# Optimization experiments

Hardware: AMD Instinct MI355X
Metric: run time of the kernel (lower is better)

The kernel has to match this reference:

```python
import jax, jax.numpy as jnp
import numpy as np

NUM_HEADS = 8  # from init_kwargs

def _conv1x1(x, W, b):
    # x: [B, Cin, H, W], W: [Cout, Cin], b: [Cout]  (nn.Conv2d kernel_size=1)
    return jnp.einsum('bchw,oc->bohw', x, W) + b[None, :, None, None]

def setup_inputs() -> dict:
    key = jax.random.key(0)
    ks = jax.random.split(key, 9)
    B, C, H, W = 8, 256, 32, 32
    Ck, Cv, Co = 256, 256, 256
    s = 1.0 / np.sqrt(C)
    return {
        'x':  jax.random.normal(ks[0], (B, C, H, W), dtype=jnp.float32),
        'Wq': jax.random.normal(ks[1], (Ck, C), dtype=jnp.float32) * s,
        'bq': jax.random.normal(ks[2], (Ck,), dtype=jnp.float32) * 0.02,
        'Wk': jax.random.normal(ks[3], (Ck, C), dtype=jnp.float32) * s,
        'bk': jax.random.normal(ks[4], (Ck,), dtype=jnp.float32) * 0.02,
        'Wv': jax.random.normal(ks[5], (Cv, C), dtype=jnp.float32) * s,
        'bv': jax.random.normal(ks[6], (Cv,), dtype=jnp.float32) * 0.02,
        'Wo': jax.random.normal(ks[7], (Co, Cv), dtype=jnp.float32) * s,
        'bo': jax.random.normal(ks[8], (Co,), dtype=jnp.float32) * 0.02,
    }

def reference(x, Wq, bq, Wk, bk, Wv, bv, Wo, bo):
    B, C, H, W = x.shape
    q = _conv1x1(x, Wq, bq)  # [B, Ck, H, W]
    k = _conv1x1(x, Wk, bk)  # [B, Ck, H, W]
    v = _conv1x1(x, Wv, bv)  # [B, Cv, H, W]
    nh = NUM_HEADS
    dk = q.shape[1] // nh
    dv = v.shape[1] // nh
    N = H * W
    # split heads, flatten spatial dims into sequence
    q = q.reshape(B, nh, dk, N) * (dk ** -0.5)
    k = k.reshape(B, nh, dk, N)
    v = v.reshape(B, nh, dv, N)
    logits = jnp.einsum('bhdn,bhdm->bhnm', q, k)        # [B, nh, N, N]
    attn = jax.nn.softmax(logits, axis=-1)
    o = jnp.einsum('bhnm,bhdm->bhdn', attn, v)           # [B, nh, dv, N]
    o = o.reshape(B, nh * dv, H, W)
    return _conv1x1(o, Wo, bo)                           # [B, Co, H, W]
```

## Files before the change

kernel.cpp:

```cpp
#include <hip/hip_runtime.h>
#include <math.h>

typedef unsigned short u16;
typedef __attribute__((ext_vector_type(8))) unsigned short u16x8;
typedef __attribute__((ext_vector_type(8))) short s16x8;
typedef __attribute__((ext_vector_type(4))) float f32x4;

#define QK_SCALE (0.17677669529663687f * 1.4426950408889634f)

__device__ __forceinline__ unsigned cvt2(float lo, float hi) {
  unsigned r;
  asm("v_cvt_pk_bf16_f32 %0, %1, %2" : "=v"(r) : "v"(lo), "v"(hi));
  return r;
}
__device__ __forceinline__ u16 f2bf(float f) { return (u16)cvt2(f, f); }
__device__ __forceinline__ u16x8 ld16(const void* p) { u16x8 v; __builtin_memcpy(&v, p, 16); return v; }
__device__ __forceinline__ void st16(void* p, u16x8 v) { __builtin_memcpy(p, &v, 16); }
__device__ __forceinline__ void st16s(void* p, s16x8 v) { __builtin_memcpy(p, &v, 16); }
__device__ __forceinline__ void st4(void* p, unsigned v) { __builtin_memcpy(p, &v, 4); }
__device__ __forceinline__ void st8(void* p, unsigned lo, unsigned hi) {
  unsigned long long v = ((unsigned long long)hi << 32) | (unsigned long long)lo;
  __builtin_memcpy(p, &v, 8);
}
__device__ __forceinline__ f32x4 ldf4(const void* p) { f32x4 v; __builtin_memcpy(&v, p, 16); return v; }
__device__ __forceinline__ void stf4(void* p, f32x4 v) { __builtin_memcpy(p, &v, 16); }
__device__ __forceinline__ s16x8 frag16(const void* p) { s16x8 v; __builtin_memcpy(&v, p, 16); return v; }
__device__ __forceinline__ s16x8 pack8(f32x4 lo, f32x4 hi) {
  union { unsigned u[4]; s16x8 s; } c;
  c.u[0] = cvt2(lo.x, lo.y); c.u[1] = cvt2(lo.z, lo.w);
  c.u[2] = cvt2(hi.x, hi.y); c.u[3] = cvt2(hi.z, hi.w);
  return c.s;
}

__global__ __launch_bounds__(256) void r22_qkv(
    const float* __restrict__ x,
    const float* __restrict__ Wq, const float* __restrict__ bq,
    const float* __restrict__ Wk, const float* __restrict__ bk,
    const float* __restrict__ Wv, const float* __restrict__ bv,
    u16* __restrict__ qo, u16* __restrict__ ko, u16* __restrict__ vo)
{
  __shared__ u16 xt[64][264];
  __shared__ u16 wlds[192][40];

  const int t = threadIdx.x;
  const int ntile = blockIdx.x, hp = blockIdx.y, b = blockIdx.z;
  const int n0 = ntile * 64, h0 = hp * 2;
  const int w = t >> 6, lane = t & 63, l15 = lane & 15, quad = lane >> 4;
  const int oct = t & 7;

  {
    const int i = t & 15, co = t >> 4;
    const float* xb = x + ((size_t)b * 256 + co) * 1024 + n0 + i * 4;
    const int msk = (i & 7) << 3;
#pragma unroll
    for (int p = 0; p < 16; ++p) {
      const f32x4 a = ldf4(xb + (size_t)p * 16 * 1024);
      const int c = p * 16 + co;
#pragma unroll
      for (int j = 0; j < 4; ++j)
        xt[i * 4 + j][(c ^ msk)] = f2bf(a[j]);
    }
  }

  f32x4 acc[12];
#pragma unroll
  for (int i = 0; i < 12; ++i) acc[i] = (f32x4){0.f, 0.f, 0.f, 0.f};

  for (int ks = 0; ks < 8; ++ks) {
    __syncthreads();
    {
#pragma unroll
      for (int u = 0; u < 6; ++u) {
        const int row = (u * 256 + t) >> 3;
        const int m = row >> 6, hh = (row >> 5) & 1, rr = row & 31;
        const float* M = (m == 0) ? Wq : (m == 1) ? Wk : Wv;
        const f32x4 a = ldf4(M + (size_t)((h0 + hh) * 32 + rr) * 256
                             + ks * 32 + oct * 4);
        st8(&wlds[row][oct * 4], cvt2(a.x, a.y), cvt2(a.z, a.w));
      }
    }
    __syncthreads();

    const int nrow = w * 16 + l15;
    const s16x8 bfrag = frag16(
        &xt[nrow][(ks * 32 + quad * 8) ^ (((nrow >> 2) & 7) << 3)]);
#pragma unroll
    for (int mt = 0; mt < 12; ++mt) {
      const s16x8 af = frag16(&wlds[mt * 16 + l15][quad * 8]);
      acc[mt] = __builtin_amdgcn_mfma_f32_16x16x32_bf16(af, bfrag, acc[mt], 0, 0, 0);
    }
  }

  const int n = n0 + w * 16 + l15;
  const int sig = n & 127;
  const int ntn = sig >> 4, q4 = (sig >> 2) & 3, rn = sig & 3;
  const int nperm = (n & ~127) | ((ntn >> 1) << 5) | (q4 << 3) | ((ntn & 1) << 2) | rn;
#pragma unroll
  for (int hh = 0; hh < 2; ++hh) {
    const int h = h0 + hh;
    const size_t bh = (size_t)(b * 8 + h);
    u16* qrow = qo + (bh * 1024 + n) * 32;
    u16* krow = ko + (bh * 1024 + n) * 32;
#pragma unroll
    for (int half = 0; half < 2; ++half) {
      const int d0 = half * 16 + quad * 4;
      const f32x4 aq = acc[0 + hh * 2 + half];
      const f32x4 ak = acc[4 + hh * 2 + half];
      const f32x4 av = acc[8 + hh * 2 + half];
      st4(qrow + d0,     cvt2((aq.x + bq[h * 32 + d0 + 0]) * QK_SCALE,
                              (aq.y + bq[h * 32 + d0 + 1]) * QK_SCALE));
      st4(qrow + d0 + 2, cvt2((aq.z + bq[h * 32 + d0 + 2]) * QK_SCALE,
                              (aq.w + bq[h * 32 + d0 + 3]) * QK_SCALE));
      st4(krow + d0,     cvt2(ak.x + bk[h * 32 + d0 + 0],
                              ak.y + bk[h * 32 + d0 + 1]));
      st4(krow + d0 + 2, cvt2(ak.z + bk[h * 32 + d0 + 2],
                              ak.w + bk[h * 32 + d0 + 3]));
#pragma unroll
      for (int rr = 0; rr < 4; ++rr) {
        const int d = d0 + rr;
        vo[(bh * 32 + d) * 1024 + nperm] = f2bf(av[rr] + bv[h * 32 + d]);
      }
    }
  }
}

__global__ __launch_bounds__(256) void r22_attn(
    const u16* __restrict__ qw, const u16* __restrict__ kw,
    const u16* __restrict__ vw, float* __restrict__ out)
{
  __shared__ u16 klds[128][40];
  __shared__ u16 vlds[32][136];

  const int t = threadIdx.x;
  const int qtile = blockIdx.x;
  const int bh = blockIdx.y;
  const int w = t >> 6, lane = t & 63, l15 = lane & 15, quad = lane >> 4;

  const s16x8 qfrag = frag16(
      qw + ((size_t)bh * 1024 + qtile * 64 + w * 16 + l15) * 32 + quad * 8);

  const u16* kbase = kw + ((size_t)bh * 1024 + (t >> 1)) * 32 + (t & 1) * 16;
  const u16* vbase = vw + ((size_t)bh * 32 + (t >> 3)) * 1024 + (t & 7) * 16;

  u16x8 gk0 = ld16(kbase), gk1 = ld16(kbase + 8);
  u16x8 gv0 = ld16(vbase), gv1 = ld16(vbase + 8);

  f32x4 o0 = {0.f, 0.f, 0.f, 0.f}, o1 = {0.f, 0.f, 0.f, 0.f};
  float mrun = -1e30f, lrun = 0.f;

  for (int kb = 0; kb < 8; ++kb) {
    if (kb) __syncthreads();
    st16(&klds[t >> 1][(t & 1) * 16], gk0);
    st16(&klds[t >> 1][(t & 1) * 16 + 8], gk1);
    st16(&vlds[t >> 3][(t & 7) * 16], gv0);
    st16(&vlds[t >> 3][(t & 7) * 16 + 8], gv1);
    if (kb < 7) {
      const u16* kn = kbase + (size_t)(kb + 1) * (128 * 32);
      const u16* vn = vbase + (size_t)(kb + 1) * 128;
      gk0 = ld16(kn); gk1 = ld16(kn + 8);
      gv0 = ld16(vn); gv1 = ld16(vn + 8);
    }
    __syncthreads();

    f32x4 s[8];
    const f32x4 zz = {0.f, 0.f, 0.f, 0.f};
#pragma unroll
    for (int nt2 = 0; nt2 < 8; ++nt2) {
      const s16x8 kf = frag16(&klds[nt2 * 16 + l15][quad * 8]);
      s[nt2] = __builtin_amdgcn_mfma_f32_16x16x32_bf16(kf, qfrag, zz, 0, 0, 0);
    }

    float mx = fmaxf(fmaxf(s[0][0], s[0][1]), fmaxf(s[0][2], s[0][3]));
#pragma unroll
    for (int nt2 = 1; nt2 < 8; ++nt2)
      mx = fmaxf(mx, fmaxf(fmaxf(s[nt2][0], s[nt2][1]),
                           fmaxf(s[nt2][2], s[nt2][3])));
    mx = fmaxf(mx, __shfl_xor(mx, 16));
    mx = fmaxf(mx, __shfl_xor(mx, 32));
    const float mnew = fmaxf(mrun, mx);
    const float alpha = exp2f(mrun - mnew);
    float rs = 0.f;
#pragma unroll
    for (int nt2 = 0; nt2 < 8; ++nt2) {
#pragma unroll
      for (int r = 0; r < 4; ++r) {
        s[nt2][r] = exp2f(s[nt2][r] - mnew);
        rs += s[nt2][r];
      }
    }
    rs += __shfl_xor(rs, 16);
    rs += __shfl_xor(rs, 32);
    lrun = lrun * alpha + rs;
    mrun = mnew;
#pragma unroll
    for (int r = 0; r < 4; ++r) { o0[r] *= alpha; o1[r] *= alpha; }

#pragma unroll
    for (int ks = 0; ks < 4; ++ks) {
      const s16x8 pf  = pack8(s[2 * ks], s[2 * ks + 1]);
      const s16x8 vf0 = frag16(&vlds[l15][ks * 32 + quad * 8]);
      const s16x8 vf1 = frag16(&vlds[16 + l15][ks * 32 + quad * 8]);
      o0 = __builtin_amdgcn_mfma_f32_16x16x32_bf16(vf0, pf, o0, 0, 0, 0);
      o1 = __builtin_amdgcn_mfma_f32_16x16x32_bf16(vf1, pf, o1, 0, 0, 0);
    }
  }

  const float inv = 1.0f / lrun;
  const int b = bh >> 3, hh = bh & 7;
  float* obase = out + ((size_t)b * 256 + hh * 32) * 1024
               + qtile * 64 + w * 16 + l15;
#pragma unroll
  for (int r = 0; r < 4; ++r) {
    obase[(size_t)(quad * 4 + r) * 1024]      = o0[r] * inv;
    obase[(size_t)(16 + quad * 4 + r) * 1024] = o1[r] * inv;
  }
}

__global__ __launch_bounds__(256) void r22_oproj(
    const float* __restrict__ Wo, const float* __restrict__ bo,
    float* __restrict__ out)
{
  __shared__ u16 o2t[32][264];
  __shared__ u16 wl3[2][256][40];

  const int t = threadIdx.x;
  const int nt = blockIdx.x, b = blockIdx.y;
  const int w = t >> 6, lane = t & 63, l15 = lane & 15, quad = lane >> 4;
  const int oct = t & 7;

  {
    const int co = t >> 3;
    const float* ob = out + ((size_t)b * 256 + co) * 1024 + nt * 32 + oct * 4;
    const int msk = oct << 3;
#pragma unroll
    for (int p = 0; p < 8; ++p) {
      const f32x4 a = ldf4(ob + (size_t)p * 32 * 1024);
      const int c = p * 32 + co;
#pragma unroll
      for (int j = 0; j < 4; ++j)
        o2t[oct * 4 + j][(c ^ msk)] = f2bf(a[j]);
    }
  }

  auto stage_wo = [&](int ks, int buf) {
#pragma unroll
    for (int u = 0; u < 8; ++u) {
      const int row = u * 32 + (t >> 3);
      const f32x4 a = ldf4(Wo + (size_t)row * 256 + ks * 32 + oct * 4);
      st8(&wl3[buf][row][oct * 4], cvt2(a.x, a.y), cvt2(a.z, a.w));
    }
  };

  stage_wo(0, 0);
  __syncthreads();

  f32x4 acc[4][2];
#pragma unroll
  for (int mt = 0; mt < 4; ++mt) {
    acc[mt][0] = (f32x4){0.f, 0.f, 0.f, 0.f};
    acc[mt][1] = (f32x4){0.f, 0.f, 0.f, 0.f};
  }

  for (int ks = 0; ks < 8; ++ks) {
    if (ks < 7) stage_wo(ks + 1, (ks + 1) & 1);
    const s16x8 b0 = frag16(
        &o2t[l15][(ks * 32 + quad * 8) ^ (((l15 >> 2) & 7) << 3)]);
    const s16x8 b1 = frag16(
        &o2t[16 + l15][(ks * 32 + quad * 8) ^ ((((16 + l15) >> 2) & 7) << 3)]);
#pragma unroll
    for (int mt = 0; mt < 4; ++mt) {
      const s16x8 af = frag16(&wl3[ks & 1][w * 64 + mt * 16 + l15][quad * 8]);
      acc[mt][0] = __builtin_amdgcn_mfma_f32_16x16x32_bf16(af, b0, acc[mt][0], 0, 0, 0);
      acc[mt][1] = __builtin_amdgcn_mfma_f32_16x16x32_bf16(af, b1, acc[mt][1], 0, 0, 0);
    }
    __syncthreads();
  }

#pragma unroll
  for (int mt = 0; mt < 4; ++mt) {
#pragma unroll
    for (int r = 0; r < 4; ++r) {
      const int oc = w * 64 + mt * 16 + quad * 4 + r;
      const float bov = bo[oc];
      out[((size_t)b * 256 + oc) * 1024 + nt * 32 + l15]      = acc[mt][0][r] + bov;
      out[((size_t)b * 256 + oc) * 1024 + nt * 32 + 16 + l15] = acc[mt][1][r] + bov;
    }
  }
}

extern "C" void kernel_launch(void* const* d_in, const int* in_sizes, int n_in,
                              void* d_out, int out_size, void* d_ws, size_t ws_size,
                              hipStream_t stream) {
  (void)in_sizes; (void)n_in; (void)out_size; (void)ws_size;
  const float* x  = (const float*)d_in[0];
  const float* Wq = (const float*)d_in[1];
  const float* bq = (const float*)d_in[2];
  const float* Wk = (const float*)d_in[3];
  const float* bk = (const float*)d_in[4];
  const float* Wv = (const float*)d_in[5];
  const float* bv = (const float*)d_in[6];
  const float* Wo = (const float*)d_in[7];
  const float* bo = (const float*)d_in[8];
  float* out = (float*)d_out;

  char* ws = (char*)d_ws;
  u16* qw = (u16*)(ws);
  u16* kw = (u16*)(ws + (4u << 20));
  u16* vw = (u16*)(ws + (8u << 20));

  r22_qkv<<<dim3(16, 4, 8), 256, 0, stream>>>(
      x, Wq, bq, Wk, bk, Wv, bv, qw, kw, vw);
  r22_attn<<<dim3(16, 64), 256, 0, stream>>>(qw, kw, vw, out);
  r22_oproj<<<dim3(32, 8), 256, 0, stream>>>(Wo, bo, out);
}
```

Baseline: 132.4 us.

## Halve per-block work in QKV and out-projection kernels, prefetch weights via registers

The QKV projection now handles one head per block instead of two, doubling its grid. The output projection now handles 16 columns instead of 32, also doubling its grid. Both kernels load the next k-slice of weights into registers while the current MFMAs run, replacing the old direct global-to-LDS staging and the double-buffered LDS. The aim is more blocks to fill the many CUs of the MI355X and some overlap of weight loads with compute. The cost is that the x/o tile gets reloaded and transposed by twice as many blocks, and weights are refetched more often.

```diff
diff --git a/kernel.cpp b/kernel.cpp
--- a/kernel.cpp
+++ b/kernel.cpp
@@ -16,14 +16,12 @@
 __device__ __forceinline__ u16 f2bf(float f) { return (u16)cvt2(f, f); }
 __device__ __forceinline__ u16x8 ld16(const void* p) { u16x8 v; __builtin_memcpy(&v, p, 16); return v; }
 __device__ __forceinline__ void st16(void* p, u16x8 v) { __builtin_memcpy(p, &v, 16); }
-__device__ __forceinline__ void st16s(void* p, s16x8 v) { __builtin_memcpy(p, &v, 16); }
 __device__ __forceinline__ void st4(void* p, unsigned v) { __builtin_memcpy(p, &v, 4); }
 __device__ __forceinline__ void st8(void* p, unsigned lo, unsigned hi) {
   unsigned long long v = ((unsigned long long)hi << 32) | (unsigned long long)lo;
   __builtin_memcpy(p, &v, 8);
 }
 __device__ __forceinline__ f32x4 ldf4(const void* p) { f32x4 v; __builtin_memcpy(&v, p, 16); return v; }
-__device__ __forceinline__ void stf4(void* p, f32x4 v) { __builtin_memcpy(p, &v, 16); }
 __device__ __forceinline__ s16x8 frag16(const void* p) { s16x8 v; __builtin_memcpy(&v, p, 16); return v; }
 __device__ __forceinline__ s16x8 pack8(f32x4 lo, f32x4 hi) {
   union { unsigned u[4]; s16x8 s; } c;
@@ -32,7 +30,7 @@
   return c.s;
 }
 
-__global__ __launch_bounds__(256) void r22_qkv(
+__global__ __launch_bounds__(256) void r23_qkv(
     const float* __restrict__ x,
     const float* __restrict__ Wq, const float* __restrict__ bq,
     const float* __restrict__ Wk, const float* __restrict__ bk,
@@ -40,11 +38,11 @@
     u16* __restrict__ qo, u16* __restrict__ ko, u16* __restrict__ vo)
 {
   __shared__ u16 xt[64][264];
-  __shared__ u16 wlds[192][40];
+  __shared__ u16 wlds[96][40];
 
   const int t = threadIdx.x;
-  const int ntile = blockIdx.x, hp = blockIdx.y, b = blockIdx.z;
-  const int n0 = ntile * 64, h0 = hp * 2;
+  const int ntile = blockIdx.x, h = blockIdx.y, b = blockIdx.z;
+  const int n0 = ntile * 64;
   const int w = t >> 6, lane = t & 63, l15 = lane & 15, quad = lane >> 4;
   const int oct = t & 7;
 
@@ -62,32 +60,51 @@
     }
   }
 
-  f32x4 acc[12];
-#pragma unroll
-  for (int i = 0; i < 12; ++i) acc[i] = (f32x4){0.f, 0.f, 0.f, 0.f};
+  const int rr = t >> 3;
+  const float* wsrc[3];
+  wsrc[0] = Wq + (size_t)(h * 32 + rr) * 256 + oct * 4;
+  wsrc[1] = Wk + (size_t)(h * 32 + rr) * 256 + oct * 4;
+  wsrc[2] = Wv + (size_t)(h * 32 + rr) * 256 + oct * 4;
+  unsigned wreg[3][2];
+#pragma unroll
+  for (int u = 0; u < 3; ++u) {
+    const f32x4 a = ldf4(wsrc[u]);
+    wreg[u][0] = cvt2(a.x, a.y); wreg[u][1] = cvt2(a.z, a.w);
+  }
+
+  f32x4 acc[6];
+#pragma unroll
+  for (int i = 0; i < 6; ++i) acc[i] = (f32x4){0.f, 0.f, 0.f, 0.f};
+
+  const int nrow = w * 16 + l15;
+  const int bmsk = ((nrow >> 2) & 7) << 3;
 
   for (int ks = 0; ks < 8; ++ks) {
     __syncthreads();
-    {
-#pragma unroll
-      for (int u = 0; u < 6; ++u) {
-        const int row = (u * 256 + t) >> 3;
-        const int m = row >> 6, hh = (row >> 5) & 1, rr = row & 31;
-        const float* M = (m == 0) ? Wq : (m == 1) ? Wk : Wv;
-        const f32x4 a = ldf4(M + (size_t)((h0 + hh) * 32 + rr) * 256
-                             + ks * 32 + oct * 4);
-        st8(&wlds[row][oct * 4], cvt2(a.x, a.y), cvt2(a.z, a.w));
-      }
-    }
-    __syncthreads();
-
-    const int nrow = w * 16 + l15;
-    const s16x8 bfrag = frag16(
-        &xt[nrow][(ks * 32 + quad * 8) ^ (((nrow >> 2) & 7) << 3)]);
-#pragma unroll
-    for (int mt = 0; mt < 12; ++mt) {
+#pragma unroll
+    for (int u = 0; u < 3; ++u)
+      st8(&wlds[u * 32 + rr][oct * 4], wreg[u][0], wreg[u][1]);
+    __syncthreads();
+
+    f32x4 nx[3];
+    if (ks < 7) {
+#pragma unroll
+      for (int u = 0; u < 3; ++u) nx[u] = ldf4(wsrc[u] + (ks + 1) * 32);
+    }
+
+    const s16x8 bfrag = frag16(&xt[nrow][(ks * 32 + quad * 8) ^ bmsk]);
+#pragma unroll
+    for (int mt = 0; mt < 6; ++mt) {
       const s16x8 af = frag16(&wlds[mt * 16 + l15][quad * 8]);
       acc[mt] = __builtin_amdgcn_mfma_f32_16x16x32_bf16(af, bfrag, acc[mt], 0, 0, 0);
+    }
+
+    if (ks < 7) {
+#pragma unroll
+      for (int u = 0; u < 3; ++u) {
+        wreg[u][0] = cvt2(nx[u].x, nx[u].y);
+        wreg[u][1] = cvt2(nx[u].z, nx[u].w);
+      }
     }
   }
 
@@ -95,36 +112,32 @@
   const int sig = n & 127;
   const int ntn = sig >> 4, q4 = (sig >> 2) & 3, rn = sig & 3;
   const int nperm = (n & ~127) | ((ntn >> 1) << 5) | (q4 << 3) | ((ntn & 1) << 2) | rn;
-#pragma unroll
-  for (int hh = 0; hh < 2; ++hh) {
-    const int h = h0 + hh;
-    const size_t bh = (size_t)(b * 8 + h);
-    u16* qrow = qo + (bh * 1024 + n) * 32;
-    u16* krow = ko + (bh * 1024 + n) * 32;
-#pragma unroll
-    for (int half = 0; half < 2; ++half) {
-      const int d0 = half * 16 + quad * 4;
-      const f32x4 aq = acc[0 + hh * 2 + half];
-      const f32x4 ak = acc[4 + hh * 2 + half];
-      const f32x4 av = acc[8 + hh * 2 + half];
-      st4(qrow + d0,     cvt2((aq.x + bq[h * 32 + d0 + 0]) * QK_SCALE,
-                              (aq.y + bq[h * 32 + d0 + 1]) * QK_SCALE));
-      st4(qrow + d0 + 2, cvt2((aq.z + bq[h * 32 + d0 + 2]) * QK_SCALE,
-                              (aq.w + bq[h * 32 + d0 + 3]) * QK_SCALE));
-      st4(krow + d0,     cvt2(ak.x + bk[h * 32 + d0 + 0],
-                              ak.y + bk[h * 32 + d0 + 1]));
-      st4(krow + d0 + 2, cvt2(ak.z + bk[h * 32 + d0 + 2],
-                              ak.w + bk[h * 32 + d0 + 3]));
-#pragma unroll
-      for (int rr = 0; rr < 4; ++rr) {
-        const int d = d0 + rr;
-        vo[(bh * 32 + d) * 1024 + nperm] = f2bf(av[rr] + bv[h * 32 + d]);
-      }
-    }
-  }
-}
-
-__global__ __launch_bounds__(256) void r22_attn(
+  const size_t bh = (size_t)(b * 8 + h);
+  u16* qrow = qo + (bh * 1024 + n) * 32;
+  u16* krow = ko + (bh * 1024 + n) * 32;
+#pragma unroll
+  for (int half = 0; half < 2; ++half) {
+    const int d0 = half * 16 + quad * 4;
+    const f32x4 aq = acc[0 + half];
+    const f32x4 ak = acc[2 + half];
+    const f32x4 av = acc[4 + half];
+    st4(qrow + d0,     cvt2((aq.x + bq[h * 32 + d0 + 0]) * QK_SCALE,
+                            (aq.y + bq[h * 32 + d0 + 1]) * QK_SCALE));
+    st4(qrow + d0 + 2, cvt2((aq.z + bq[h * 32 + d0 + 2]) * QK_SCALE,
+                            (aq.w + bq[h * 32 + d0 + 3]) * QK_SCALE));
+    st4(krow + d0,     cvt2(ak.x + bk[h * 32 + d0 + 0],
+                            ak.y + bk[h * 32 + d0 + 1]));
+    st4(krow + d0 + 2, cvt2(ak.z + bk[h * 32 + d0 + 2],
+                            ak.w + bk[h * 32 + d0 + 3]));
+#pragma unroll
+    for (int rr2 = 0; rr2 < 4; ++rr2) {
+      const int d = d0 + rr2;
+      vo[(bh * 32 + d) * 1024 + nperm] = f2bf(av[rr2] + bv[h * 32 + d]);
+    }
+  }
+}
+
+__global__ __launch_bounds__(256) void r23_attn(
     const u16* __restrict__ qw, const u16* __restrict__ kw,
     const u16* __restrict__ vw, float* __restrict__ out)
 {
@@ -216,12 +229,12 @@
   }
 }
 
-__global__ __launch_bounds__(256) void r22_oproj(
+__global__ __launch_bounds__(256) void r23_oproj(
     const float* __restrict__ Wo, const float* __restrict__ bo,
     float* __restrict__ out)
 {
-  __shared__ u16 o2t[32][264];
-  __shared__ u16 wl3[2][256][40];
+  __shared__ u16 o2t[16][264];
+  __shared__ u16 wl3[256][40];
 
   const int t = threadIdx.x;
   const int nt = blockIdx.x, b = blockIdx.y;
@@ -229,51 +242,62 @@
   const int oct = t & 7;
 
   {
-    const int co = t >> 3;
-    const float* ob = out + ((size_t)b * 256 + co) * 1024 + nt * 32 + oct * 4;
-    const int msk = oct << 3;
-#pragma unroll
-    for (int p = 0; p < 8; ++p) {
-      const f32x4 a = ldf4(ob + (size_t)p * 32 * 1024);
-      const int c = p * 32 + co;
+    const int nq = t & 3, co = t >> 2;
+    const float* ob = out + ((size_t)b * 256 + co) * 1024 + nt * 16 + nq * 4;
+    const int msk = nq << 3;
+#pragma unroll
+    for (int p = 0; p < 4; ++p) {
+      const f32x4 a = ldf4(ob + (size_t)p * 64 * 1024);
+      const int c = p * 64 + co;
 #pragma unroll
       for (int j = 0; j < 4; ++j)
-        o2t[oct * 4 + j][(c ^ msk)] = f2bf(a[j]);
-    }
-  }
-
-  auto stage_wo = [&](int ks, int buf) {
-#pragma unroll
-    for (int u = 0; u < 8; ++u) {
-      const int row = u * 32 + (t >> 3);
-      const f32x4 a = ldf4(Wo + (size_t)row * 256 + ks * 32 + oct * 4);
-      st8(&wl3[buf][row][oct * 4], cvt2(a.x, a.y), cvt2(a.z, a.w));
-    }
-  };
-
-  stage_wo(0, 0);
-  __syncthreads();
-
-  f32x4 acc[4][2];
-#pragma unroll
-  for (int mt = 0; mt < 4; ++mt) {
-    acc[mt][0] = (f32x4){0.f, 0.f, 0.f, 0.f};
-    acc[mt][1] = (f32x4){0.f, 0.f, 0.f, 0.f};
-  }
+        o2t[nq * 4 + j][(c ^ msk)] = f2bf(a[j]);
+    }
+  }
+
+  const int rr = t >> 3;
+  const float* wsrc = Wo + (size_t)rr * 256 + oct * 4;
+  unsigned wreg[8][2];
+#pragma unroll
+  for (int u = 0; u < 8; ++u) {
+    const f32x4 a = ldf4(wsrc + (size_t)u * 32 * 256);
+    wreg[u][0] = cvt2(a.x, a.y); wreg[u][1] = cvt2(a.z, a.w);
+  }
+
+  f32x4 acc[4];
+#pragma unroll
+  for (int mt = 0; mt < 4; ++mt) acc[mt] = (f32x4){0.f, 0.f, 0.f, 0.f};
+
+  const int bmsk = ((l15 >> 2) & 7) << 3;
 
   for (int ks = 0; ks < 8; ++ks) {
-    if (ks < 7) stage_wo(ks + 1, (ks + 1) & 1);
-    const s16x8 b0 = frag16(
-        &o2t[l15][(ks * 32 + quad * 8) ^ (((l15 >> 2) & 7) << 3)]);
-    const s16x8 b1 = frag16(
-        &o2t[16 + l15][(ks * 32 + quad * 8) ^ ((((16 + l15) >> 2) & 7) << 3)]);
+    __syncthreads();
+#pragma unroll
+    for (int u = 0; u < 8; ++u)
+      st8(&wl3[u * 32 + rr][oct * 4], wreg[u][0], wreg[u][1]);
+    __syncthreads();
+
+    f32x4 nx[8];
+    if (ks < 7) {
+#pragma unroll
+      for (int u = 0; u < 8; ++u)
+        nx[u] = ldf4(wsrc + (size_t)u * 32 * 256 + (ks + 1) * 32);
+    }
+
+    const s16x8 b0 = frag16(&o2t[l15][(ks * 32 + quad * 8) ^ bmsk]);
 #pragma unroll
     for (int mt = 0; mt < 4; ++mt) {
-      const s16x8 af = frag16(&wl3[ks & 1][w * 64 + mt * 16 + l15][quad * 8]);
-      acc[mt][0] = __builtin_amdgcn_mfma_f32_16x16x32_bf16(af, b0, acc[mt][0], 0, 0, 0);
-      acc[mt][1] = __builtin_amdgcn_mfma_f32_16x16x32_bf16(af, b1, acc[mt][1], 0, 0, 0);
-    }
-    __syncthreads();
+      const s16x8 af = frag16(&wl3[w * 64 + mt * 16 + l15][quad * 8]);
+      acc[mt] = __builtin_amdgcn_mfma_f32_16x16x32_bf16(af, b0, acc[mt], 0, 0, 0);
+    }
+
+    if (ks < 7) {
+#pragma unroll
+      for (int u = 0; u < 8; ++u) {
+        wreg[u][0] = cvt2(nx[u].x, nx[u].y);
+        wreg[u][1] = cvt2(nx[u].z, nx[u].w);
+      }
+    }
   }
 
 #pragma unroll
@@ -281,9 +305,7 @@
 #pragma unroll
     for (int r = 0; r < 4; ++r) {
       const int oc = w * 64 + mt * 16 + quad * 4 + r;
-      const float bov = bo[oc];
-      out[((size_t)b * 256 + oc) * 1024 + nt * 32 + l15]      = acc[mt][0][r] + bov;
-      out[((size_t)b * 256 + oc) * 1024 + nt * 32 + 16 + l15] = acc[mt][1][r] + bov;
+      out[((size_t)b * 256 + oc) * 1024 + nt * 16 + l15] = acc[mt][r] + bo[oc];
     }
   }
 }
@@ -308,8 +330,8 @@
   u16* kw = (u16*)(ws + (4u << 20));
   u16* vw = (u16*)(ws + (8u << 20));
 
-  r22_qkv<<<dim3(16, 4, 8), 256, 0, stream>>>(
+  r23_qkv<<<dim3(16, 8, 8), 256, 0, stream>>>(
       x, Wq, bq, Wk, bk, Wv, bv, qw, kw, vw);
-  r22_attn<<<dim3(16, 64), 256, 0, stream>>>(qw, kw, vw, out);
-  r22_oproj<<<dim3(32, 8), 256, 0, stream>>>(Wo, bo, out);
-}
+  r23_attn<<<dim3(16, 64), 256, 0, stream>>>(qw, kw, vw, out);
+  r23_oproj<<<dim3(64, 8), 256, 0, stream>>>(Wo, bo, out);
+}
```

Result: slower. 135.5 us (+2.3%).
